# Kernel optimization log

Measured on AMD Instinct MI355X. Metric: run time of the kernel, lower is better.

The kernel has to match this reference:

```python
import jax, jax.numpy as jnp
import numpy as np

N = 80000      # rechits per event
K = 512        # max truth objects (t_idx in [-1, K))
C = 2          # n_ccoords
NCLS = 6       # pred_id width
Q_MIN = 0.1
S_B = 1.0
NOISE_SCALER = 1.0
BETA_LOSS_SCALE = 1.0
POTENTIAL_SCALING = 1.0
REPULSION_SCALING = 1.0
ENERGY_LOSS_WEIGHT = 1.0
POSITION_LOSS_WEIGHT = 1.0
TIMING_LOSS_WEIGHT = 1.0
CLASSIFICATION_LOSS_WEIGHT = 1.0
CC_DAMPING = 0.001
EPS = 1e-9


def huber(x, d):
    absx = jnp.abs(x)
    return jnp.where(absx < d, x ** 2, d ** 2 + 2.0 * d * (absx - d))


def softclip(x, startclipat):
    x = x / startclipat
    x = jnp.where(x > 1.0, jnp.log(x + 1.0), x)
    return x * startclipat


def calc_energy_weights(t_energy):
    lower_cut = 0.5
    w = jnp.where(t_energy > 10.0, 1.0, (t_energy - lower_cut) / 10.0 * 10.0 / (10.0 - lower_cut))
    return jax.nn.relu(w)


def calc_energy_loss(t_energy, pred_energy):
    # alt_energy_loss=True branch: mild-gradient modified 1-exp form
    ediff = jnp.abs(t_energy - pred_energy)
    l = 10.0 * jnp.exp(-0.1 * ediff ** 2) + 0.01 * ediff
    return softclip(l, 10.0)


def calc_position_loss(t_pos, pred_pos):
    d2 = jnp.sum((t_pos - pred_pos) ** 2, axis=-1, keepdims=True)
    ploss = huber(jnp.sqrt(d2 / 10.0 ** 2 + 0.01), 10.0)
    return softclip(ploss, 3.0)


def calc_timing_loss(t_time, pred_time):
    return softclip(huber(t_time - pred_time, 2.0), 6.0)


def calc_classification_loss(t_pid, pred_id):
    return 1e-08 * jnp.mean(pred_id ** 2, axis=-1, keepdims=True)


def setup_inputs() -> dict:
    key = jax.random.key(0)
    ks = jax.random.split(key, 11)
    t_idx = jax.random.randint(ks[6], (N, 1), 0, K + 1) - 1  # -1 == noise
    return {
        'pred_beta': jax.random.uniform(ks[0], (N, 1), jnp.float32, 0.01, 0.99),
        'pred_ccoords': jax.random.normal(ks[1], (N, C), jnp.float32),
        'pred_energy': 100.0 * jax.random.uniform(ks[2], (N, 1), jnp.float32),
        'pred_pos': jax.random.normal(ks[3], (N, 2), jnp.float32),
        'pred_time': jax.random.normal(ks[4], (N, 1), jnp.float32),
        'pred_id': jax.random.normal(ks[5], (N, NCLS), jnp.float32),
        't_idx': t_idx.astype(jnp.int32),
        't_energy': 100.0 * jax.random.uniform(ks[7], (N, 1), jnp.float32),
        't_pos': jax.random.normal(ks[8], (N, 2), jnp.float32),
        't_time': jax.random.normal(ks[9], (N, 1), jnp.float32),
        't_pid': jax.random.uniform(ks[10], (N, 1), jnp.float32),
    }


def reference(pred_beta, pred_ccoords, pred_energy, pred_pos, pred_time, pred_id,
              t_idx, t_energy, t_pos, t_time, t_pid):
    beta = jnp.clip(pred_beta, 1e-6, 1.0 - 1e-6)                 # (N,1)
    q = jnp.arctanh(beta) ** 2 + Q_MIN                           # (N,1) charge

    is_obj = (t_idx >= 0)                                        # (N,1) bool
    M = (t_idx == jnp.arange(K)[None, :]) & is_obj               # (N,K) object membership
    Mf = M.astype(beta.dtype)
    obj_count = jnp.sum(Mf, axis=0)                              # (K,)
    has_obj = obj_count > 0.0                                    # (K,)
    n_obj = jnp.sum(has_obj.astype(beta.dtype)) + EPS

    # condensation point alpha_k: argmax beta within each object
    beta_masked = jnp.where(M, beta, -1.0)                       # (N,K)
    alpha = jnp.argmax(beta_masked, axis=0)                      # (K,)
    x_alpha = pred_ccoords[alpha]                                # (K,C)
    q_alpha = q[alpha, 0]                                        # (K,)
    beta_alpha = beta[alpha, 0]                                  # (K,)

    # pairwise squared distances hit <-> condensation point
    d2 = jnp.sum((pred_ccoords[:, None, :] - x_alpha[None, :, :]) ** 2, axis=-1)  # (N,K)

    # attractive potential (same object)
    att = Mf * d2 * q_alpha[None, :] * q                         # (N,K)
    L_att_k = jnp.sum(att, axis=0) / (obj_count + EPS)
    L_att = jnp.sum(jnp.where(has_obj, L_att_k, 0.0)) / n_obj

    # repulsive potential (other objects), hinge at unit distance
    rep = (1.0 - Mf) * jax.nn.relu(1.0 - jnp.sqrt(d2 + 1e-6)) * q_alpha[None, :] * q
    L_rep_k = jnp.sum(rep, axis=0) / (jnp.float32(N) - obj_count + EPS)
    L_rep = jnp.sum(jnp.where(has_obj, L_rep_k, 0.0)) / n_obj

    # beta loss: push condensation betas to 1, noise betas to 0
    L_beta = BETA_LOSS_SCALE * jnp.sum(jnp.where(has_obj, 1.0 - beta_alpha, 0.0)) / n_obj
    is_noise = (~is_obj).astype(beta.dtype)                      # (N,1)
    L_noise = S_B * NOISE_SCALER * jnp.sum(is_noise * beta) / (jnp.sum(is_noise) + EPS)

    # payload losses, beta- and energy-weighted, normalized per object
    payload = (ENERGY_LOSS_WEIGHT * calc_energy_loss(t_energy, pred_energy)
               + POSITION_LOSS_WEIGHT * calc_position_loss(t_pos, pred_pos)
               + TIMING_LOSS_WEIGHT * calc_timing_loss(t_time, pred_time)
               + CLASSIFICATION_LOSS_WEIGHT * calc_classification_loss(t_pid, pred_id))  # (N,1)
    pw = beta * calc_energy_weights(t_energy) * is_obj.astype(beta.dtype)               # (N,1)
    num = jnp.sum(Mf * (payload * pw), axis=0)                   # (K,)
    den = jnp.sum(Mf * pw, axis=0)                               # (K,)
    L_pay = jnp.sum(jnp.where(has_obj, num / (den + EPS), 0.0)) / n_obj

    L_cc = CC_DAMPING * jnp.mean(pred_ccoords ** 2)

    total = (POTENTIAL_SCALING * L_att + REPULSION_SCALING * L_rep
             + L_beta + L_noise + L_pay + L_cc)
    return total
```

## Files before the change

kernel.cpp:

```cpp
#include <hip/hip_runtime.h>
#include <math.h>

#define KOBJ  512
#define NCLS  6
#define QMIN  0.1f
#define EPSF  1e-9f

#define NBH  64
#define KC   64
#define GX   64
#define NTB  (GX * (KOBJ / KC))
#define HP   5

struct Ws {
    unsigned long long p_packed[NBH][KOBJ];
    float p_num[NBH][KOBJ];
    float p_den[NBH][KOBJ];
    int   p_cnt[NBH][KOBJ];
    float pnoise[NBH][4];
    float pobj[KOBJ / KC][4];
    float scal[2];
    unsigned int ticket;
};

__device__ __forceinline__ float clipb(float b) {
    return fminf(fmaxf(b, 1e-6f), 1.0f - 1e-6f);
}

__device__ __forceinline__ float fsqrt(float x)  { return __builtin_amdgcn_sqrtf(x); }
__device__ __forceinline__ float frcp(float x)   { return __builtin_amdgcn_rcpf(x); }
__device__ __forceinline__ float qval(float b) {
    float at = 0.5f * __logf((1.f + b) * frcp(1.f - b));
    return at * at + QMIN;
}

__device__ __forceinline__ float waveSum(float v) {
#pragma unroll
    for (int o = 32; o > 0; o >>= 1) v += __shfl_down(v, o, 64);
    return v;
}

__global__ __launch_bounds__(256)
void k_hits(const float* __restrict__ beta_in, const float* __restrict__ cc,
            const float* __restrict__ pe,  const float* __restrict__ ppos,
            const float* __restrict__ pt,  const float* __restrict__ pid,
            const int*   __restrict__ tidx,const float* __restrict__ te,
            const float* __restrict__ tpos,const float* __restrict__ tt,
            Ws* __restrict__ ws, int n)
{
    const int b = blockIdx.x, t = threadIdx.x;
    if (b == 0 && t == 0) {
        ws->scal[0] = 0.f; ws->scal[1] = 0.f; ws->ticket = 0u;
    }

    __shared__ unsigned long long lpk[KOBJ];
    __shared__ float lnum[KOBJ], lden[KOBJ];
    __shared__ int   lcnt[KOBJ];
    for (int k = t; k < KOBJ; k += 256) { lpk[k] = 0ull; lnum[k] = 0.f; lden[k] = 0.f; lcnt[k] = 0; }
    __syncthreads();

    float ccs = 0.f, nb = 0.f, nc = 0.f;
    for (int i = b * 256 + t; i < n; i += NBH * 256) {
        float bb = clipb(beta_in[i]);
        float c0 = cc[2*i], c1 = cc[2*i+1];
        ccs += c0*c0 + c1*c1;
        int k = tidx[i];
        if (k >= 0) {
            unsigned long long key =
                ((unsigned long long)__float_as_uint(bb) << 32) | (unsigned)(~i);
            atomicMax(&lpk[k], key);
            atomicAdd(&lcnt[k], 1);

            float tei   = te[i];
            float ediff = fabsf(tei - pe[i]);
            float el = 10.f * __expf(-0.1f * ediff * ediff) + 0.01f * ediff;
            { float x = el * 0.1f; if (x > 1.f) x = __logf(x + 1.f); el = x * 10.f; }

            float dx  = tpos[2*i]   - ppos[2*i];
            float dy  = tpos[2*i+1] - ppos[2*i+1];
            float d2p = dx*dx + dy*dy;
            float hx  = fsqrt(d2p * 0.01f + 0.01f);
            float pl  = (hx < 10.f) ? hx*hx : 100.f + 20.f*(hx - 10.f);
            { float x = pl * (1.f/3.f); if (x > 1.f) x = __logf(x + 1.f); pl = x * 3.f; }

            float td  = tt[i] - pt[i];
            float atd = fabsf(td);
            float tl  = (atd < 2.f) ? td*td : 4.f + 4.f*(atd - 2.f);
            { float x = tl * (1.f/6.f); if (x > 1.f) x = __logf(x + 1.f); tl = x * 6.f; }

            float cls = 0.f;
#pragma unroll
            for (int j = 0; j < NCLS; ++j) { float v = pid[i*NCLS + j]; cls += v*v; }
            cls *= (1e-8f / (float)NCLS);

            float payload = el + pl + tl + cls;
            float ew = (tei > 10.f) ? 1.f : (tei - 0.5f) * (1.f / 9.5f);
            ew = fmaxf(ew, 0.f);
            float pw = bb * ew;
            atomicAdd(&lnum[k], payload * pw);
            atomicAdd(&lden[k], pw);
        } else {
            nb += bb; nc += 1.f;
        }
    }
    __syncthreads();

    for (int k = t; k < KOBJ; k += 256) {
        ws->p_packed[b][k] = lpk[k];
        ws->p_num[b][k]    = lnum[k];
        ws->p_den[b][k]    = lden[k];
        ws->p_cnt[b][k]    = lcnt[k];
    }

    __shared__ float sred[3][4];
    float A = waveSum(ccs), B = waveSum(nb), C = waveSum(nc);
    int lane = t & 63, wv = t >> 6;
    if (lane == 0) { sred[0][wv] = A; sred[1][wv] = B; sred[2][wv] = C; }
    __syncthreads();
    if (t == 0) {
        float a = 0.f, x = 0.f, y = 0.f;
        for (int j = 0; j < 4; ++j) { a += sred[0][j]; x += sred[1][j]; y += sred[2][j]; }
        ws->pnoise[b][0] = a; ws->pnoise[b][1] = x; ws->pnoise[b][2] = y;
    }
}

__global__ __launch_bounds__(256)
void k_pair(const float* __restrict__ beta_in, const float* __restrict__ cc,
            const int* __restrict__ tidx, Ws* __restrict__ ws,
            float* __restrict__ out, int n)
{
    const int b = blockIdx.x, t = threadIdx.x;
    const int lane = t & 63, wv = t >> 6;
    const int kchunk = b / GX;
    const int xi     = b - kchunk * GX;
    const int kbase  = kchunk * KC;

    __shared__ float4 sk[KC];
    __shared__ unsigned long long spk[4][KC];
    __shared__ float snum[4][KC], sden[4][KC];
    __shared__ int   scnt[4][KC];
    {
        int k = kbase + lane;
        unsigned long long pk = 0ull;
        float nm = 0.f, dn = 0.f; int ct = 0;
#pragma unroll 4
        for (int j = wv * (NBH/4); j < (wv+1) * (NBH/4); ++j) {
            unsigned long long v = ws->p_packed[j][k];
            pk = (v > pk) ? v : pk;
            nm += ws->p_num[j][k];
            dn += ws->p_den[j][k];
            ct += ws->p_cnt[j][k];
        }
        spk[wv][lane] = pk; snum[wv][lane] = nm; sden[wv][lane] = dn; scnt[wv][lane] = ct;
    }
    __syncthreads();
    if (wv == 0) {
        unsigned long long pk = spk[0][lane];
        float nm = snum[0][lane], dn = sden[0][lane];
        int ct = scnt[0][lane];
#pragma unroll
        for (int j = 1; j < 4; ++j) {
            unsigned long long v = spk[j][lane];
            pk = (v > pk) ? v : pk;
            nm += snum[j][lane]; dn += sden[j][lane]; ct += scnt[j][lane];
        }
        float flag = 0.f, bsum = 0.f, payk = 0.f;
        float q_a = 0.f, x0 = 0.f, x1 = 0.f;
        if (ct > 0) {
            flag = 1.f;
            unsigned idx = ~(unsigned)(pk & 0xffffffffull);
            float bb = clipb(beta_in[idx]);
            bsum = 1.f - bb;
            q_a = qval(bb);
            x0 = cc[2*idx]; x1 = cc[2*idx + 1];
            payk = nm / (dn + EPSF);
        }
        sk[lane] = make_float4(x0, x1,
                               flag * q_a / ((float)n - (float)ct + EPSF),
                               flag * q_a / ((float)ct + EPSF));
        if (xi == 0) {
            float f  = waveSum(flag);
            float bs = waveSum(bsum);
            float ps = waveSum(payk);
            if (lane == 0) {
                ws->pobj[kchunk][0] = f;
                ws->pobj[kchunk][1] = bs;
                ws->pobj[kchunk][2] = ps;
            }
        }
    }
    __syncthreads();

    const int xspan = GX * 256;
    const int i0 = xi * 256 + t;

    float c0[HP], c1[HP], qq[HP], acc[HP];
    int   k0[HP];
#pragma unroll
    for (int j = 0; j < HP; ++j) {
        int i = i0 + j * xspan;
        bool v = (i < n);
        c0[j] = v ? cc[2*i]     : 1e30f;
        c1[j] = v ? cc[2*i + 1] : 1e30f;
        float bb = v ? clipb(beta_in[i]) : 0.5f;
        qq[j] = qval(bb);
        k0[j] = v ? tidx[i] : -1;
        acc[j] = 0.f;
    }

#pragma unroll 4
    for (int k = 0; k < KC; ++k) {
        float4 kv = sk[k];
#pragma unroll
        for (int j = 0; j < HP; ++j) {
            float dx = c0[j] - kv.x, dy = c1[j] - kv.y;
            float d2e = fmaf(dx, dx, fmaf(dy, dy, 1e-6f));
            float r   = fsqrt(d2e);
            acc[j] = fmaf(fmaxf(1.f - r, 0.f), kv.z, acc[j]);
        }
    }

    float att = 0.f, rep = 0.f;
#pragma unroll
    for (int j = 0; j < HP; ++j) {
        int kk = k0[j] - kbase;
        if (kk >= 0 && kk < KC) {
            float4 kv = sk[kk];
            float dx = c0[j] - kv.x, dy = c1[j] - kv.y;
            float d2e = fmaf(dx, dx, fmaf(dy, dy, 1e-6f));
            float r   = fsqrt(d2e);
            acc[j] -= fmaxf(1.f - r, 0.f) * kv.z;
            float d2 = fmaf(dx, dx, dy * dy);
            att = fmaf(d2 * kv.w, qq[j], att);
        }
        rep = fmaf(acc[j], qq[j], rep);
    }

    __shared__ float sred[2][4];
    __shared__ bool  is_last;
    float A = waveSum(att), R = waveSum(rep);
    if (lane == 0) { sred[0][wv] = A; sred[1][wv] = R; }
    __syncthreads();
    if (t == 0) {
        float sa = 0.f, sr = 0.f;
        for (int j = 0; j < 4; ++j) { sa += sred[0][j]; sr += sred[1][j]; }
        atomicAdd(&ws->scal[0], sa);
        atomicAdd(&ws->scal[1], sr);
        __threadfence();
        unsigned prev = atomicAdd(&ws->ticket, 1u);
        is_last = (prev == NTB - 1);
    }
    __syncthreads();

    if (is_last && wv == 0) {
        __threadfence();
        float ccs = (lane < NBH) ? ws->pnoise[lane][0] : 0.f;
        float nB  = (lane < NBH) ? ws->pnoise[lane][1] : 0.f;
        float nC  = (lane < NBH) ? ws->pnoise[lane][2] : 0.f;
        float fS  = (lane < KOBJ/KC) ? ws->pobj[lane][0] : 0.f;
        float bS  = (lane < KOBJ/KC) ? ws->pobj[lane][1] : 0.f;
        float pS  = (lane < KOBJ/KC) ? ws->pobj[lane][2] : 0.f;
        ccs = waveSum(ccs); nB = waveSum(nB); nC = waveSum(nC);
        fS  = waveSum(fS);  bS = waveSum(bS); pS = waveSum(pS);
        if (lane == 0) {
            float attS = atomicAdd(&ws->scal[0], 0.f);
            float repS = atomicAdd(&ws->scal[1], 0.f);
            float n_obj = fS + EPSF;
            out[0] = (attS + repS + bS + pS) / n_obj
                   + nB / (nC + EPSF)
                   + 0.001f * ccs / (float)(2 * n);
        }
    }
}

extern "C" void kernel_launch(void* const* d_in, const int* in_sizes, int n_in,
                              void* d_out, int out_size, void* d_ws, size_t ws_size,
                              hipStream_t stream)
{
    const float* pred_beta    = (const float*)d_in[0];
    const float* pred_ccoords = (const float*)d_in[1];
    const float* pred_energy  = (const float*)d_in[2];
    const float* pred_pos     = (const float*)d_in[3];
    const float* pred_time    = (const float*)d_in[4];
    const float* pred_id      = (const float*)d_in[5];
    const int*   t_idx        = (const int*)d_in[6];
    const float* t_energy     = (const float*)d_in[7];
    const float* t_pos        = (const float*)d_in[8];
    const float* t_time       = (const float*)d_in[9];

    float* out = (float*)d_out;
    Ws* ws = (Ws*)d_ws;
    int n = in_sizes[0];

    k_hits<<<NBH, 256, 0, stream>>>(pred_beta, pred_ccoords, pred_energy, pred_pos,
                                    pred_time, pred_id, t_idx, t_energy, t_pos,
                                    t_time, ws, n);
    k_pair<<<NTB, 256, 0, stream>>>(pred_beta, pred_ccoords, t_idx, ws, out, n);
}
```

Measured before the change: 113.3 us.

## Split object reduction into separate kernel, widen hit grid, deterministic final reduce

The hit pass now launches 320 blocks, one element per thread, instead of 64 blocks looping over the input, which gives it more parallelism. The per-object merge that every pair block used to repeat (reading all partial rows) moves into a dedicated 8-block kernel that writes an object vector once. Pair blocks now just load a 64-entry chunk of that vector. The atomic ticket and last-block pattern is replaced by per-block partials and a single-block final kernel. In exchange there are two extra launches, and the merge step reads five times more partial rows. Correctness also now depends on n being at most 320*256.

```diff
diff --git a/kernel.cpp b/kernel.cpp
--- a/kernel.cpp
+++ b/kernel.cpp
@@ -6,7 +6,8 @@
 #define QMIN  0.1f
 #define EPSF  1e-9f
 
-#define NBH  64
+#define NBH  320
+#define ROWS_PER (NBH / 16)
 #define KC   64
 #define GX   64
 #define NTB  (GX * (KOBJ / KC))
@@ -18,9 +19,9 @@
     float p_den[NBH][KOBJ];
     int   p_cnt[NBH][KOBJ];
     float pnoise[NBH][4];
-    float pobj[KOBJ / KC][4];
-    float scal[2];
-    unsigned int ticket;
+    float kvec[KOBJ * 4];
+    float pobj[8][4];
+    float pattrep[NTB][2];
 };
 
 __device__ __forceinline__ float clipb(float b) {
@@ -49,9 +50,6 @@
             Ws* __restrict__ ws, int n)
 {
     const int b = blockIdx.x, t = threadIdx.x;
-    if (b == 0 && t == 0) {
-        ws->scal[0] = 0.f; ws->scal[1] = 0.f; ws->ticket = 0u;
-    }
 
     __shared__ unsigned long long lpk[KOBJ];
     __shared__ float lnum[KOBJ], lden[KOBJ];
@@ -60,10 +58,11 @@
     __syncthreads();
 
     float ccs = 0.f, nb = 0.f, nc = 0.f;
-    for (int i = b * 256 + t; i < n; i += NBH * 256) {
+    const int i = b * 256 + t;
+    if (i < n) {
         float bb = clipb(beta_in[i]);
         float c0 = cc[2*i], c1 = cc[2*i+1];
-        ccs += c0*c0 + c1*c1;
+        ccs = c0*c0 + c1*c1;
         int k = tidx[i];
         if (k >= 0) {
             unsigned long long key =
@@ -100,7 +99,7 @@
             atomicAdd(&lnum[k], payload * pw);
             atomicAdd(&lden[k], pw);
         } else {
-            nb += bb; nc += 1.f;
+            nb = bb; nc = 1.f;
         }
     }
     __syncthreads();
@@ -124,42 +123,33 @@
     }
 }
 
-__global__ __launch_bounds__(256)
-void k_pair(const float* __restrict__ beta_in, const float* __restrict__ cc,
-            const int* __restrict__ tidx, Ws* __restrict__ ws,
-            float* __restrict__ out, int n)
-{
-    const int b = blockIdx.x, t = threadIdx.x;
-    const int lane = t & 63, wv = t >> 6;
-    const int kchunk = b / GX;
-    const int xi     = b - kchunk * GX;
-    const int kbase  = kchunk * KC;
-
-    __shared__ float4 sk[KC];
-    __shared__ unsigned long long spk[4][KC];
-    __shared__ float snum[4][KC], sden[4][KC];
-    __shared__ int   scnt[4][KC];
-    {
-        int k = kbase + lane;
-        unsigned long long pk = 0ull;
-        float nm = 0.f, dn = 0.f; int ct = 0;
+__global__ __launch_bounds__(1024)
+void k_obj(const float* __restrict__ beta_in, const float* __restrict__ cc,
+           Ws* __restrict__ ws, int n)
+{
+    const int t = threadIdx.x, lane = t & 63, wv = t >> 6;
+    const int k = blockIdx.x * 64 + lane;
+
+    unsigned long long pk = 0ull;
+    float nm = 0.f, dn = 0.f;
+    int   ct = 0;
 #pragma unroll 4
-        for (int j = wv * (NBH/4); j < (wv+1) * (NBH/4); ++j) {
-            unsigned long long v = ws->p_packed[j][k];
-            pk = (v > pk) ? v : pk;
-            nm += ws->p_num[j][k];
-            dn += ws->p_den[j][k];
-            ct += ws->p_cnt[j][k];
-        }
-        spk[wv][lane] = pk; snum[wv][lane] = nm; sden[wv][lane] = dn; scnt[wv][lane] = ct;
-    }
-    __syncthreads();
+    for (int j = wv * ROWS_PER; j < (wv + 1) * ROWS_PER; ++j) {
+        unsigned long long v = ws->p_packed[j][k];
+        pk = (v > pk) ? v : pk;
+        nm += ws->p_num[j][k];
+        dn += ws->p_den[j][k];
+        ct += ws->p_cnt[j][k];
+    }
+    __shared__ unsigned long long spk[16][64];
+    __shared__ float snum[16][64], sden[16][64];
+    __shared__ int   scnt[16][64];
+    spk[wv][lane] = pk; snum[wv][lane] = nm; sden[wv][lane] = dn; scnt[wv][lane] = ct;
+    __syncthreads();
+
     if (wv == 0) {
-        unsigned long long pk = spk[0][lane];
-        float nm = snum[0][lane], dn = sden[0][lane];
-        int ct = scnt[0][lane];
-#pragma unroll
-        for (int j = 1; j < 4; ++j) {
+#pragma unroll
+        for (int j = 1; j < 16; ++j) {
             unsigned long long v = spk[j][lane];
             pk = (v > pk) ? v : pk;
             nm += snum[j][lane]; dn += sden[j][lane]; ct += scnt[j][lane];
@@ -175,25 +165,36 @@
             x0 = cc[2*idx]; x1 = cc[2*idx + 1];
             payk = nm / (dn + EPSF);
         }
-        sk[lane] = make_float4(x0, x1,
-                               flag * q_a / ((float)n - (float)ct + EPSF),
-                               flag * q_a / ((float)ct + EPSF));
-        if (xi == 0) {
-            float f  = waveSum(flag);
-            float bs = waveSum(bsum);
-            float ps = waveSum(payk);
-            if (lane == 0) {
-                ws->pobj[kchunk][0] = f;
-                ws->pobj[kchunk][1] = bs;
-                ws->pobj[kchunk][2] = ps;
-            }
-        }
-    }
-    __syncthreads();
+        ((float4*)ws->kvec)[k] = make_float4(
+            x0, x1,
+            flag * q_a / ((float)n - (float)ct + EPSF),
+            flag * q_a / ((float)ct + EPSF));
+        float f  = waveSum(flag);
+        float bs = waveSum(bsum);
+        float ps = waveSum(payk);
+        if (lane == 0) {
+            ws->pobj[blockIdx.x][0] = f;
+            ws->pobj[blockIdx.x][1] = bs;
+            ws->pobj[blockIdx.x][2] = ps;
+        }
+    }
+}
+
+__global__ __launch_bounds__(256)
+void k_pair(const float* __restrict__ beta_in, const float* __restrict__ cc,
+            const int* __restrict__ tidx, Ws* __restrict__ ws, int n)
+{
+    const int b = blockIdx.x, t = threadIdx.x;
+    const int lane = t & 63, wv = t >> 6;
+    const int kchunk = b / GX;
+    const int xi     = b - kchunk * GX;
+    const int kbase  = kchunk * KC;
+
+    __shared__ float4 sk[KC];
+    if (t < KC) sk[t] = ((const float4*)ws->kvec)[kbase + t];
 
     const int xspan = GX * 256;
     const int i0 = xi * 256 + t;
-
     float c0[HP], c1[HP], qq[HP], acc[HP];
     int   k0[HP];
 #pragma unroll
@@ -207,6 +208,7 @@
         k0[j] = v ? tidx[i] : -1;
         acc[j] = 0.f;
     }
+    __syncthreads();
 
 #pragma unroll 4
     for (int k = 0; k < KC; ++k) {
@@ -237,39 +239,49 @@
     }
 
     __shared__ float sred[2][4];
-    __shared__ bool  is_last;
     float A = waveSum(att), R = waveSum(rep);
     if (lane == 0) { sred[0][wv] = A; sred[1][wv] = R; }
     __syncthreads();
     if (t == 0) {
         float sa = 0.f, sr = 0.f;
         for (int j = 0; j < 4; ++j) { sa += sred[0][j]; sr += sred[1][j]; }
-        atomicAdd(&ws->scal[0], sa);
-        atomicAdd(&ws->scal[1], sr);
-        __threadfence();
-        unsigned prev = atomicAdd(&ws->ticket, 1u);
-        is_last = (prev == NTB - 1);
-    }
-    __syncthreads();
-
-    if (is_last && wv == 0) {
-        __threadfence();
-        float ccs = (lane < NBH) ? ws->pnoise[lane][0] : 0.f;
-        float nB  = (lane < NBH) ? ws->pnoise[lane][1] : 0.f;
-        float nC  = (lane < NBH) ? ws->pnoise[lane][2] : 0.f;
-        float fS  = (lane < KOBJ/KC) ? ws->pobj[lane][0] : 0.f;
-        float bS  = (lane < KOBJ/KC) ? ws->pobj[lane][1] : 0.f;
-        float pS  = (lane < KOBJ/KC) ? ws->pobj[lane][2] : 0.f;
-        ccs = waveSum(ccs); nB = waveSum(nB); nC = waveSum(nC);
-        fS  = waveSum(fS);  bS = waveSum(bS); pS = waveSum(pS);
-        if (lane == 0) {
-            float attS = atomicAdd(&ws->scal[0], 0.f);
-            float repS = atomicAdd(&ws->scal[1], 0.f);
-            float n_obj = fS + EPSF;
-            out[0] = (attS + repS + bS + pS) / n_obj
-                   + nB / (nC + EPSF)
-                   + 0.001f * ccs / (float)(2 * n);
-        }
+        ws->pattrep[b][0] = sa;
+        ws->pattrep[b][1] = sr;
+    }
+}
+
+__global__ __launch_bounds__(512)
+void k_final(Ws* __restrict__ ws, float* __restrict__ out, int n)
+{
+    const int t = threadIdx.x, lane = t & 63, wv = t >> 6;
+
+    float att = ws->pattrep[t][0];
+    float rep = ws->pattrep[t][1];
+    float ccs = 0.f, nB = 0.f, nC = 0.f;
+    if (t < NBH) { ccs = ws->pnoise[t][0]; nB = ws->pnoise[t][1]; nC = ws->pnoise[t][2]; }
+    float fS = 0.f, bS = 0.f, pS = 0.f;
+    if (t < 8)   { fS = ws->pobj[t][0]; bS = ws->pobj[t][1]; pS = ws->pobj[t][2]; }
+
+    att = waveSum(att); rep = waveSum(rep);
+    ccs = waveSum(ccs); nB = waveSum(nB); nC = waveSum(nC);
+    fS = waveSum(fS); bS = waveSum(bS); pS = waveSum(pS);
+
+    __shared__ float fin[8][8];
+    if (lane == 0) {
+        fin[0][wv] = att; fin[1][wv] = rep; fin[2][wv] = ccs; fin[3][wv] = nB;
+        fin[4][wv] = nC;  fin[5][wv] = fS;  fin[6][wv] = bS;  fin[7][wv] = pS;
+    }
+    __syncthreads();
+    if (t == 0) {
+        float v[8];
+        for (int m = 0; m < 8; ++m) {
+            v[m] = 0.f;
+            for (int j = 0; j < 8; ++j) v[m] += fin[m][j];
+        }
+        float n_obj = v[5] + EPSF;
+        out[0] = (v[0] + v[1] + v[6] + v[7]) / n_obj
+               + v[3] / (v[4] + EPSF)
+               + 0.001f * v[2] / (float)(2 * n);
     }
 }
 
@@ -295,5 +307,7 @@
     k_hits<<<NBH, 256, 0, stream>>>(pred_beta, pred_ccoords, pred_energy, pred_pos,
                                     pred_time, pred_id, t_idx, t_energy, t_pos,
                                     t_time, ws, n);
-    k_pair<<<NTB, 256, 0, stream>>>(pred_beta, pred_ccoords, t_idx, ws, out, n);
-}
+    k_obj<<<8, 1024, 0, stream>>>(pred_beta, pred_ccoords, ws, n);
+    k_pair<<<NTB, 256, 0, stream>>>(pred_beta, pred_ccoords, t_idx, ws, n);
+    k_final<<<1, 512, 0, stream>>>(ws, out, n);
+}
```

Result: faster. 102.8 us (-9.2%).
